# Performance work log

Measured on AMD Instinct MI355X. Metric: run time of the kernel, lower is better.

Reference implementation:

```python
import jax, jax.numpy as jnp
import numpy as np

B, L, H = 256, 512, 256      # batch, seq_len, hid_dim
REL_VOCAB = 50000            # relation_input_dim
A = 100000                   # size of global action pool (len(actions))
K = 512                      # action keys per sample (padded ragged dim)
ENT_VOCAB = 40000
PAD = 0                      # entity_pad_idx


def setup_inputs() -> dict:
    key = jax.random.key(0)
    k1, k2, k3, k4, k5, k6 = jax.random.split(key, 6)
    entities = jax.random.randint(k1, (B, L), 0, ENT_VOCAB)
    relations = jax.random.randint(k2, (B, L), 0, REL_VOCAB)
    actions = jax.random.randint(k3, (A,), 0, REL_VOCAB)
    action_keys = jax.random.randint(k4, (B, K), 0, A)
    encoded = jax.random.normal(k5, (B, L, H), dtype=jnp.float32)  # opaque encoder output
    rel_emb = jax.random.normal(k6, (REL_VOCAB, H), dtype=jnp.float32) * 0.02
    return {"entities": entities, "relations": relations, "actions": actions,
            "action_keys": action_keys, "encoded": encoded, "rel_emb": rel_emb}


def reference(entities, relations, actions, action_keys, encoded, rel_emb):
    # mask-based gather of the last non-pad position per sample
    mask = (entities != PAD)                       # [B, L]
    idxs = mask.sum(axis=1) - 1                    # [B]
    enc_last = jnp.take_along_axis(
        encoded, idxs[:, None, None], axis=1).squeeze(1)  # [B, H]
    # only_relations branch: action embedding lookup for the global action pool
    action_emb = rel_emb[actions]                  # [A, H]
    # ragged (padded) per-sample gather + matvec: preds[b,k] = action_emb[keys[b,k]] . enc_last[b]
    gathered = action_emb[action_keys]             # [B, K, H]
    preds = jnp.einsum('bkh,bh->bk', gathered, enc_last)  # [B, K]
    return preds
```

## Files before the change

kernel.cpp:

```cpp
#include <hip/hip_runtime.h>

#define B 256
#define L 512
#define H 256
#define K 512
#define BINS 16
#define BINW 3125
#define STRIDE 12288

#define WS_CNT_OFF 0
#define WS_ENC_OFF 1024
#define WS_ENT_OFF (512 * 1024)

__global__ __launch_bounds__(256)
void passA_bin(const int* __restrict__ entities,
               const int* __restrict__ actions,
               const int* __restrict__ action_keys,
               const float* __restrict__ encoded,
               float* __restrict__ ws_enc,
               int* __restrict__ ws_cnt,
               uint2* __restrict__ ws_ent)
{
    const int b    = blockIdx.x;
    const int t    = threadIdx.x;
    const int lane = t & 63;
    const int wave = t >> 6;

    __shared__ int s_count;
    __shared__ int s_wcnt[4][BINS];
    __shared__ int s_wbase[4][BINS];

    if (t == 0) s_count = 0;
    if (t < 4 * BINS) ((int*)s_wcnt)[t] = 0;
    __syncthreads();

    unsigned long long m0 = __ballot(entities[b * L + t] != 0);
    unsigned long long m1 = __ballot(entities[b * L + t + 256] != 0);
    if (lane == 0) atomicAdd(&s_count, __popcll(m0) + __popcll(m1));
    __syncthreads();
    int idx = s_count - 1;
    idx = max(0, min(L - 1, idx));

    ws_enc[b * H + t] = encoded[((size_t)(b * L + idx)) * H + t];

    const int k0 = t, k1 = t + 256;
    const int r0 = actions[action_keys[b * K + k0]];
    const int r1 = actions[action_keys[b * K + k1]];
    const int bin0 = r0 / BINW;
    const int bin1 = r1 / BINW;

    const unsigned long long mlt = (lane == 63) ? 0x7FFFFFFFFFFFFFFFull
                                                : ((1ull << lane) - 1ull);
    int pos0 = 0, pos1 = 0;
    #pragma unroll
    for (int bb = 0; bb < BINS; ++bb) {
        unsigned long long ma = __ballot(bin0 == bb);
        unsigned long long mb = __ballot(bin1 == bb);
        int ca = __popcll(ma);
        int cb = __popcll(mb);
        if (lane == 0) s_wcnt[wave][bb] = ca + cb;
        if (bin0 == bb) pos0 = __popcll(ma & mlt);
        if (bin1 == bb) pos1 = ca + __popcll(mb & mlt);
    }
    __syncthreads();

    if (t < BINS) {
        int tot = 0, basew[4];
        #pragma unroll
        for (int w = 0; w < 4; ++w) { basew[w] = tot; tot += s_wcnt[w][t]; }
        int g = atomicAdd(&ws_cnt[t], tot);
        #pragma unroll
        for (int w = 0; w < 4; ++w) s_wbase[w][t] = g + basew[w];
    }
    __syncthreads();

    const int p0 = s_wbase[wave][bin0] + pos0;
    const int p1 = s_wbase[wave][bin1] + pos1;
    if (p0 < STRIDE) ws_ent[bin0 * STRIDE + p0] = make_uint2((unsigned)(b * K + k0), (unsigned)r0);
    if (p1 < STRIDE) ws_ent[bin1 * STRIDE + p1] = make_uint2((unsigned)(b * K + k1), (unsigned)r1);
}

__device__ __forceinline__ float dot4(const float4 a, const float4 b) {
    return a.x * b.x + a.y * b.y + a.z * b.z + a.w * b.w;
}

__global__ __launch_bounds__(256)
void passB_dot(const float* __restrict__ rel_emb,
               const float* __restrict__ ws_enc,
               const int* __restrict__ ws_cnt,
               const uint2* __restrict__ ws_ent,
               float* __restrict__ out)
{
    const int blk   = blockIdx.x;
    const int xcd   = blk & 7;
    const int phase = blk >> 11;
    const int slot  = (blk >> 3) & 255;
    const int bin   = xcd * 2 + phase;

    const int count = min(ws_cnt[bin], STRIDE);
    const int per_block = (count + 255) >> 8;
    const int start = slot * per_block;
    const int end   = min(count, start + per_block);

    const int t    = threadIdx.x;
    const int lane = t & 63;
    const int wave = t >> 6;
    const int gidx = wave * 4 + (lane >> 4);
    const int gl   = lane & 15;

    const uint2* ebase = ws_ent + bin * STRIDE;

    for (int p = start + gidx * 2; p < end; p += 32) {
        const bool v1 = (p + 1) < end;
        const uint2 e0 = ebase[p];
        const uint2 e1 = v1 ? ebase[p + 1] : e0;

        const float* r0 = &rel_emb[(size_t)e0.y * H];
        const float* r1 = &rel_emb[(size_t)e1.y * H];
        const float* q0 = &ws_enc[(e0.x >> 9) * H];
        const float* q1 = &ws_enc[(e1.x >> 9) * H];

        float4 a0 = *(const float4*)&r0[gl * 4];
        float4 a1 = *(const float4*)&r0[gl * 4 + 64];
        float4 a2 = *(const float4*)&r0[gl * 4 + 128];
        float4 a3 = *(const float4*)&r0[gl * 4 + 192];
        float4 b0 = *(const float4*)&r1[gl * 4];
        float4 b1 = *(const float4*)&r1[gl * 4 + 64];
        float4 b2 = *(const float4*)&r1[gl * 4 + 128];
        float4 b3 = *(const float4*)&r1[gl * 4 + 192];

        float4 ea0 = *(const float4*)&q0[gl * 4];
        float4 ea1 = *(const float4*)&q0[gl * 4 + 64];
        float4 ea2 = *(const float4*)&q0[gl * 4 + 128];
        float4 ea3 = *(const float4*)&q0[gl * 4 + 192];
        float4 eb0 = *(const float4*)&q1[gl * 4];
        float4 eb1 = *(const float4*)&q1[gl * 4 + 64];
        float4 eb2 = *(const float4*)&q1[gl * 4 + 128];
        float4 eb3 = *(const float4*)&q1[gl * 4 + 192];

        float s0 = dot4(a0, ea0) + dot4(a1, ea1) + dot4(a2, ea2) + dot4(a3, ea3);
        float s1 = dot4(b0, eb0) + dot4(b1, eb1) + dot4(b2, eb2) + dot4(b3, eb3);

        #pragma unroll
        for (int off = 1; off < 16; off <<= 1) {
            s0 += __shfl_xor(s0, off, 64);
            s1 += __shfl_xor(s1, off, 64);
        }
        if (gl == 0) {
            out[e0.x] = s0;
            if (v1) out[e1.x] = s1;
        }
    }
}

extern "C" void kernel_launch(void* const* d_in, const int* in_sizes, int n_in,
                              void* d_out, int out_size, void* d_ws, size_t ws_size,
                              hipStream_t stream)
{
    const int*   entities    = (const int*)d_in[0];
    const int*   actions     = (const int*)d_in[2];
    const int*   action_keys = (const int*)d_in[3];
    const float* encoded     = (const float*)d_in[4];
    const float* rel_emb     = (const float*)d_in[5];
    float*       out         = (float*)d_out;

    char* ws = (char*)d_ws;
    int*   ws_cnt = (int*)(ws + WS_CNT_OFF);
    float* ws_enc = (float*)(ws + WS_ENC_OFF);
    uint2* ws_ent = (uint2*)(ws + WS_ENT_OFF);

    hipMemsetAsync(ws_cnt, 0, BINS * sizeof(int), stream);

    hipLaunchKernelGGL(passA_bin, dim3(B), dim3(256), 0, stream,
                       entities, actions, action_keys, encoded,
                       ws_enc, ws_cnt, ws_ent);

    hipLaunchKernelGGL(passB_dot, dim3(BINS * 256), dim3(256), 0, stream,
                       rel_emb, ws_enc, ws_cnt, ws_ent, out);
}
```

Baseline: 30.35 us.

## Use finer relation bins with XCD-aware dynamic work stealing in dot pass

Splits relation rows into 64 narrower bins (8 per XCD) so each XCD's working set of rel_emb rows is smaller and fits better in its local L2. Blocks read their hardware XCC_ID and walk that XCD's bins in turn, taking 64-entry chunks through a global atomic work pointer instead of a fixed static partition. Each 16-lane group now handles one entry per iteration, four times per chunk. The trade-off is more ballot iterations in the binning pass (64 bins, no longer unrolled), an atomic plus two barriers per chunk, and reliance on the XCC_ID register mapping; a per-bin capacity of 2560 may also drop entries if the distribution is skewed.

```diff
diff --git a/kernel.cpp b/kernel.cpp
--- a/kernel.cpp
+++ b/kernel.cpp
@@ -4,11 +4,15 @@
 #define L 512
 #define H 256
 #define K 512
-#define BINS 16
-#define BINW 3125
-#define STRIDE 12288
+#define BINS 64
+#define BINW 782
+#define STRIDE 2560
+#define NXCD 8
+#define SUBBINS (BINS / NXCD)
+#define GRAB 64
 
 #define WS_CNT_OFF 0
+#define WS_WP_OFF  256
 #define WS_ENC_OFF 1024
 #define WS_ENT_OFF (512 * 1024)
 
@@ -31,7 +35,7 @@
     __shared__ int s_wbase[4][BINS];
 
     if (t == 0) s_count = 0;
-    if (t < 4 * BINS) ((int*)s_wcnt)[t] = 0;
+    if (t < 256) { ((int*)s_wcnt)[t] = 0; }
     __syncthreads();
 
     unsigned long long m0 = __ballot(entities[b * L + t] != 0);
@@ -52,7 +56,6 @@
     const unsigned long long mlt = (lane == 63) ? 0x7FFFFFFFFFFFFFFFull
                                                 : ((1ull << lane) - 1ull);
     int pos0 = 0, pos1 = 0;
-    #pragma unroll
     for (int bb = 0; bb < BINS; ++bb) {
         unsigned long long ma = __ballot(bin0 == bb);
         unsigned long long mb = __ballot(bin1 == bb);
@@ -88,67 +91,61 @@
 void passB_dot(const float* __restrict__ rel_emb,
                const float* __restrict__ ws_enc,
                const int* __restrict__ ws_cnt,
+               int* __restrict__ ws_wp,
                const uint2* __restrict__ ws_ent,
                float* __restrict__ out)
 {
-    const int blk   = blockIdx.x;
-    const int xcd   = blk & 7;
-    const int phase = blk >> 11;
-    const int slot  = (blk >> 3) & 255;
-    const int bin   = xcd * 2 + phase;
-
-    const int count = min(ws_cnt[bin], STRIDE);
-    const int per_block = (count + 255) >> 8;
-    const int start = slot * per_block;
-    const int end   = min(count, start + per_block);
+    int xcd;
+    asm volatile("s_getreg_b32 %0, hwreg(HW_REG_XCC_ID)" : "=s"(xcd));
+    xcd &= 7;
 
     const int t    = threadIdx.x;
     const int lane = t & 63;
     const int wave = t >> 6;
-    const int gidx = wave * 4 + (lane >> 4);
+    const int g    = lane >> 4;
     const int gl   = lane & 15;
 
-    const uint2* ebase = ws_ent + bin * STRIDE;
+    __shared__ int s_grab;
 
-    for (int p = start + gidx * 2; p < end; p += 32) {
-        const bool v1 = (p + 1) < end;
-        const uint2 e0 = ebase[p];
-        const uint2 e1 = v1 ? ebase[p + 1] : e0;
+    for (int phase = 0; phase < SUBBINS; ++phase) {
+        const int bin = xcd * SUBBINS + phase;
+        const int cnt = min(ws_cnt[bin], STRIDE);
+        const uint2* ebase = ws_ent + (size_t)bin * STRIDE;
 
-        const float* r0 = &rel_emb[(size_t)e0.y * H];
-        const float* r1 = &rel_emb[(size_t)e1.y * H];
-        const float* q0 = &ws_enc[(e0.x >> 9) * H];
-        const float* q1 = &ws_enc[(e1.x >> 9) * H];
+        for (;;) {
+            if (t == 0) s_grab = atomicAdd(&ws_wp[bin], GRAB);
+            __syncthreads();
+            const int c = s_grab;
+            __syncthreads();
+            if (c >= cnt) break;
 
-        float4 a0 = *(const float4*)&r0[gl * 4];
-        float4 a1 = *(const float4*)&r0[gl * 4 + 64];
-        float4 a2 = *(const float4*)&r0[gl * 4 + 128];
-        float4 a3 = *(const float4*)&r0[gl * 4 + 192];
-        float4 b0 = *(const float4*)&r1[gl * 4];
-        float4 b1 = *(const float4*)&r1[gl * 4 + 64];
-        float4 b2 = *(const float4*)&r1[gl * 4 + 128];
-        float4 b3 = *(const float4*)&r1[gl * 4 + 192];
+            const int pw = c + 16 * wave + g;
+            #pragma unroll
+            for (int it = 0; it < 4; ++it) {
+                const int p = pw + 4 * it;
+                const bool valid = (p < cnt);
+                const uint2 E = valid ? ebase[p] : make_uint2(0u, 0u);
 
-        float4 ea0 = *(const float4*)&q0[gl * 4];
-        float4 ea1 = *(const float4*)&q0[gl * 4 + 64];
-        float4 ea2 = *(const float4*)&q0[gl * 4 + 128];
-        float4 ea3 = *(const float4*)&q0[gl * 4 + 192];
-        float4 eb0 = *(const float4*)&q1[gl * 4];
-        float4 eb1 = *(const float4*)&q1[gl * 4 + 64];
-        float4 eb2 = *(const float4*)&q1[gl * 4 + 128];
-        float4 eb3 = *(const float4*)&q1[gl * 4 + 192];
+                const float* r = &rel_emb[(size_t)E.y * H + gl * 16];
+                const float* q = &ws_enc[(E.x >> 9) * H + gl * 16];
 
-        float s0 = dot4(a0, ea0) + dot4(a1, ea1) + dot4(a2, ea2) + dot4(a3, ea3);
-        float s1 = dot4(b0, eb0) + dot4(b1, eb1) + dot4(b2, eb2) + dot4(b3, eb3);
+                float4 r0 = *(const float4*)&r[0];
+                float4 r1 = *(const float4*)&r[4];
+                float4 r2 = *(const float4*)&r[8];
+                float4 r3 = *(const float4*)&r[12];
+                float4 q0 = *(const float4*)&q[0];
+                float4 q1 = *(const float4*)&q[4];
+                float4 q2 = *(const float4*)&q[8];
+                float4 q3 = *(const float4*)&q[12];
 
-        #pragma unroll
-        for (int off = 1; off < 16; off <<= 1) {
-            s0 += __shfl_xor(s0, off, 64);
-            s1 += __shfl_xor(s1, off, 64);
-        }
-        if (gl == 0) {
-            out[e0.x] = s0;
-            if (v1) out[e1.x] = s1;
+                float s = dot4(r0, q0) + dot4(r1, q1) + dot4(r2, q2) + dot4(r3, q3);
+
+                #pragma unroll
+                for (int off = 1; off < 16; off <<= 1)
+                    s += __shfl_xor(s, off, 64);
+
+                if (valid && gl == 0) out[E.x] = s;
+            }
         }
     }
 }
@@ -166,15 +163,16 @@
 
     char* ws = (char*)d_ws;
     int*   ws_cnt = (int*)(ws + WS_CNT_OFF);
+    int*   ws_wp  = (int*)(ws + WS_WP_OFF);
     float* ws_enc = (float*)(ws + WS_ENC_OFF);
     uint2* ws_ent = (uint2*)(ws + WS_ENT_OFF);
 
-    hipMemsetAsync(ws_cnt, 0, BINS * sizeof(int), stream);
+    hipMemsetAsync(ws, 0, 512, stream);
 
     hipLaunchKernelGGL(passA_bin, dim3(B), dim3(256), 0, stream,
                        entities, actions, action_keys, encoded,
                        ws_enc, ws_cnt, ws_ent);
 
-    hipLaunchKernelGGL(passB_dot, dim3(BINS * 256), dim3(256), 0, stream,
-                       rel_emb, ws_enc, ws_cnt, ws_ent, out);
+    hipLaunchKernelGGL(passB_dot, dim3(2048), dim3(256), 0, stream,
+                       rel_emb, ws_enc, ws_cnt, ws_wp, ws_ent, out);
 }
```

Result: slower. 115.4 us (+280.2%).
